# Performance work log

Hardware: AMD Instinct MI355X
Metric: run time of the kernel (lower is better)

Reference implementation:

```python
import jax, jax.numpy as jnp
import numpy as np

N_NODES = 100000
N_EDGES = 1600000
D_IN = 128
D_HID = 128
D_OUT = 10
N_GRAPHS = 512


def _sage_conv(x, src, dst, W_l, b_l, W_r, num_nodes):
    # PyG SAGEConv (mean aggr): out = lin_l(mean_{j in N(i)} x_j) + lin_r(x_i)
    msg = x[src]                                            # [E, D] gather
    s = jax.ops.segment_sum(msg, dst, num_segments=num_nodes)
    cnt = jax.ops.segment_sum(jnp.ones((src.shape[0], 1), x.dtype), dst,
                              num_segments=num_nodes)
    mean = s / jnp.maximum(cnt, 1.0)                        # 0 where no neighbors
    return mean @ W_l.T + b_l + x @ W_r.T


def setup_inputs() -> dict:
    key = jax.random.key(0)
    ks = jax.random.split(key, 10)
    glorot = lambda k, o, i: jax.random.normal(k, (o, i), jnp.float32) * (1.0 / np.sqrt(i))
    return {
        "x": jax.random.normal(ks[0], (N_NODES, D_IN), jnp.float32),
        "edge_index": jax.random.randint(ks[1], (2, N_EDGES), 0, N_NODES, jnp.int64),
        "batch": jnp.sort(jax.random.randint(ks[2], (N_NODES,), 0, N_GRAPHS, jnp.int64)),
        "W1_l": glorot(ks[3], D_HID, D_IN),
        "b1": jnp.zeros((D_HID,), jnp.float32),
        "W1_r": glorot(ks[4], D_HID, D_IN),
        "W2_l": glorot(ks[5], D_HID, D_HID),
        "b2": jnp.zeros((D_HID,), jnp.float32),
        "W2_r": glorot(ks[6], D_HID, D_HID),
        "Wf": glorot(ks[7], D_OUT, D_HID),
        "bf": jnp.zeros((D_OUT,), jnp.float32),
    }


def reference(x, edge_index, batch, W1_l, b1, W1_r, W2_l, b2, W2_r, Wf, bf):
    src, dst = edge_index[0], edge_index[1]
    n = x.shape[0]
    h = jax.nn.relu(_sage_conv(x, src, dst, W1_l, b1, W1_r, n))
    h = jax.nn.relu(_sage_conv(h, src, dst, W2_l, b2, W2_r, n))
    # global_mean_pool over graph ids
    gsum = jax.ops.segment_sum(h, batch, num_segments=N_GRAPHS)
    gcnt = jax.ops.segment_sum(jnp.ones((n, 1), h.dtype), batch, num_segments=N_GRAPHS)
    g = gsum / jnp.maximum(gcnt, 1.0)
    logits = g @ Wf.T + bf
    return jax.nn.log_softmax(logits, axis=-1)
```

## Files before the change

kernel.cpp:

```cpp
#include <hip/hip_runtime.h>
#include <hip/hip_bf16.h>

#define N_NODES 100000
#define N_EDGES 1600000
#define N_GRAPHS 512
#define NB 256
#define NPB 391
#define CHUNK 6250
#define STAGE 7680

typedef __attribute__((ext_vector_type(8))) short short8;
typedef __attribute__((ext_vector_type(4))) float f32x4;
typedef __attribute__((ext_vector_type(2))) float f32x2;

__device__ __forceinline__ float b2f(ushort u) {
    union { unsigned int i; float f; } c; c.i = ((unsigned int)u) << 16; return c.f;
}
__device__ __forceinline__ float blo(unsigned int u) {
    union { unsigned int i; float f; } c; c.i = u << 16; return c.f;
}
__device__ __forceinline__ float bhi(unsigned int u) {
    union { unsigned int i; float f; } c; c.i = u & 0xffff0000u; return c.f;
}
__device__ __forceinline__ ushort f2b(float f) {
    union { float f; unsigned int i; } c; c.f = f;
    unsigned int r = (c.i + 0x7fffu + ((c.i >> 16) & 1u)) >> 16;
    return (ushort)r;
}
__device__ __forceinline__ int idx_at(const void* p, long i, int f) {
    return f ? (int)((const long long*)p)[i] : ((const int*)p)[i];
}

__global__ __launch_bounds__(256) void k_detect(const unsigned int* __restrict__ xw,
                                                const unsigned int* __restrict__ ew,
                                                const int* __restrict__ bw,
                                                int* __restrict__ flags) {
    __shared__ int cf, ce, cb;
    int t = threadIdx.x;
    if (t == 0) { cf = 0; ce = 0; cb = 0; }
    __syncthreads();
    unsigned int w = xw[t];
    unsigned int e = (w >> 7) & 0xffu;
    if (e >= 110u && e <= 130u) atomicAdd(&cf, 1);
    if (t < 128) {
        if (ew[2 * t + 1] != 0u) atomicAdd(&ce, 1);
        if (bw[99001 + 2 * t] != 0) atomicAdd(&cb, 1);
    }
    __syncthreads();
    if (t == 0) {
        flags[0] = (cf >= 128) ? 1 : 0;
        flags[1] = (ce == 0) ? 1 : 0;
        flags[2] = (cb == 0) ? 1 : 0;
    }
}

__global__ __launch_bounds__(256) void k_prep(const void* __restrict__ ei,
                                              const void* __restrict__ x,
                                              ushort* __restrict__ xbf,
                                              unsigned int* __restrict__ xf8,
                                              const void* W1l, const void* W1r,
                                              const void* W2l, const void* W2r,
                                              const void* b1,  const void* b2,
                                              ushort* __restrict__ wbf,
                                              int* __restrict__ blkcnt,
                                              const int* __restrict__ flags) {
    int b = blockIdx.x, t = threadIdx.x;
    if (b < NB) {
        __shared__ int h[NB];
        int f = flags[1];
        for (int j = t; j < NB; j += 256) h[j] = 0;
        __syncthreads();
        int lo = b * CHUNK, hi = lo + CHUNK;
        for (int e = lo + t; e < hi; e += 256) {
            int d = idx_at(ei, (long)N_EDGES + e, f);
            atomicAdd(&h[d / NPB], 1);
        }
        __syncthreads();
        if (t < NB) blkcnt[b * NB + t] = h[t];
    } else if (b < NB + 2048) {
        bool f32src = (flags[0] == 0);
        int vb = b - NB;
        const long nG = (long)N_NODES * 128 / 4;
        for (long g = (long)vb * 256 + t; g < nG; g += 2048L * 256) {
            float v0, v1, v2, v3;
            if (f32src) {
                float4 vv = ((const float4*)x)[g];
                v0 = vv.x; v1 = vv.y; v2 = vv.z; v3 = vv.w;
                unsigned int lo = (unsigned int)f2b(v0) | ((unsigned int)f2b(v1) << 16);
                unsigned int hi = (unsigned int)f2b(v2) | ((unsigned int)f2b(v3) << 16);
                ((uint2*)xbf)[g] = make_uint2(lo, hi);
            } else {
                uint2 q = ((const uint2*)x)[g];
                v0 = blo(q.x); v1 = bhi(q.x); v2 = blo(q.y); v3 = bhi(q.y);
            }
            int r = __builtin_amdgcn_cvt_pk_fp8_f32(v0, v1, 0, false);
            r = __builtin_amdgcn_cvt_pk_fp8_f32(v2, v3, r, true);
            xf8[g] = (unsigned int)r;
        }
    } else {
        int idx = (b - NB - 2048) * 256 + t;
        if (idx >= 65792) return;
        const void* src; int off;
        if      (idx < 16384) { src = W1l; off = idx; }
        else if (idx < 32768) { src = W1r; off = idx - 16384; }
        else if (idx < 49152) { src = W2l; off = idx - 32768; }
        else if (idx < 65536) { src = W2r; off = idx - 49152; }
        else if (idx < 65664) { src = b1;  off = idx - 65536; }
        else                  { src = b2;  off = idx - 65664; }
        wbf[idx] = (flags[0] != 0) ? ((const ushort*)src)[off]
                                   : f2b(((const float*)src)[off]);
    }
}

__global__ __launch_bounds__(NB) void k_bscan(const int* __restrict__ blkcnt,
                                              int* __restrict__ bucketBase,
                                              int* __restrict__ blkbase) {
    __shared__ int s[NB];
    int t = threadIdx.x;
    int tot = 0;
    for (int blk = 0; blk < NB; ++blk) tot += blkcnt[blk * NB + t];
    s[t] = tot; __syncthreads();
    for (int off = 1; off < NB; off <<= 1) {
        int a = (t >= off) ? s[t - off] : 0;
        __syncthreads();
        s[t] += a;
        __syncthreads();
    }
    int excl = s[t] - tot;
    bucketBase[t] = excl;
    if (t == NB - 1) bucketBase[NB] = s[NB - 1];
    int run = excl;
    for (int blk = 0; blk < NB; ++blk) {
        blkbase[blk * NB + t] = run;
        run += blkcnt[blk * NB + t];
    }
}

__global__ __launch_bounds__(256) void k_bin(const void* __restrict__ ei,
                                             const int* __restrict__ blkbase,
                                             int* __restrict__ binned,
                                             const int* __restrict__ flags) {
    __shared__ int bb[NB];
    __shared__ int rank[NB];
    int t = threadIdx.x, blk = blockIdx.x;
    int f = flags[1];
    for (int j = t; j < NB; j += 256) { bb[j] = blkbase[blk * NB + j]; rank[j] = 0; }
    __syncthreads();
    int lo = blk * CHUNK, hi = lo + CHUNK;
    for (int e = lo + t; e < hi; e += 256) {
        int s = idx_at(ei, e, f);
        int d = idx_at(ei, (long)N_EDGES + e, f);
        int b = d / NPB;
        int loc = d - b * NPB;
        int r = atomicAdd(&rank[b], 1);
        binned[bb[b] + r] = s | (loc << 20);
    }
}

__global__ __launch_bounds__(256) void k_csr(const int* __restrict__ binned,
                                             const int* __restrict__ bucketBase,
                                             int* __restrict__ rowptr,
                                             int* __restrict__ csr) {
    __shared__ int cnt[400];
    __shared__ int sc[400];
    __shared__ int sh[256];
    __shared__ int stage[STAGE];
    int t = threadIdx.x, b = blockIdx.x;
    int nodeLo = b * NPB;
    int nC = N_NODES - nodeLo; if (nC > NPB) nC = NPB;
    int eBase = bucketBase[b], eEnd = bucketBase[b + 1];

    for (int j = t; j < 400; j += 256) cnt[j] = 0;
    __syncthreads();
    for (int i = eBase + t; i < eEnd; i += 256)
        atomicAdd(&cnt[binned[i] >> 20], 1);
    __syncthreads();
    int base = t * 2;
    int v0 = (base < 400) ? cnt[base] : 0;
    int v1 = (base + 1 < 400) ? cnt[base + 1] : 0;
    int ssum = v0 + v1;
    sh[t] = ssum; __syncthreads();
    for (int off = 1; off < 256; off <<= 1) {
        int a = (t >= off) ? sh[t - off] : 0;
        __syncthreads();
        sh[t] += a;
        __syncthreads();
    }
    int pre = sh[t] - ssum;
    if (base < 400) sc[base] = pre;
    if (base + 1 < 400) sc[base + 1] = pre + v0;
    __syncthreads();
    for (int j = t; j < nC; j += 256) rowptr[nodeLo + j] = eBase + sc[j];
    if (b == NB - 1) {
        if (t == 0) rowptr[N_NODES] = eEnd;
        if (t < 64) csr[N_EDGES + t] = 0;
    }
    for (int j = t; j < 400; j += 256) cnt[j] = 0;
    __syncthreads();
    for (int i = eBase + t; i < eEnd; i += 256) {
        int p = binned[i];
        int loc = p >> 20;
        int pos = sc[loc] + atomicAdd(&cnt[loc], 1);
        int srcn = p & 0xFFFFF;
        if (pos < STAGE) stage[pos] = srcn;
        else csr[eBase + pos] = srcn;
    }
    __syncthreads();
    int eCnt = eEnd - eBase; if (eCnt > STAGE) eCnt = STAGE;
    for (int j = t; j < eCnt; j += 256) csr[eBase + j] = stage[j];
}

__global__ __launch_bounds__(256) void k_agg(const unsigned int* __restrict__ x32,
                                             const int* __restrict__ rowptr,
                                             const int* __restrict__ csr,
                                             uint2* __restrict__ mout) {
    int wv = blockIdx.x * 4 + (threadIdx.x >> 6);
    int lane = threadIdx.x & 63;
    int li = lane & 31;
    int node = wv * 2 + (lane >> 5);
    if (node >= N_NODES) return;
    int beg = rowptr[node];
    int end = rowptr[node + 1];
    int deg = end - beg;
    int degO = __shfl_xor(deg, 32);
    int degmax = __builtin_amdgcn_readfirstlane(deg > degO ? deg : degO);
    float a0 = 0.f, a1 = 0.f, a2 = 0.f, a3 = 0.f;
    for (int j = 0; j < degmax; j += 32) {
        int pos = beg + j + li;
        if (pos > end - 1) pos = (deg > 0) ? end - 1 : 0;
        int vidx = csr[pos];
#pragma unroll
        for (int c = 0; c < 32; c += 8) {
            if (j + c >= degmax) break;
            unsigned int p[8];
#pragma unroll
            for (int i = 0; i < 8; ++i) {
                int idx = __shfl(vidx, (c + i) | (lane & 32));
                p[i] = x32[(long)idx * 32 + li];
            }
#pragma unroll
            for (int i = 0; i < 8; ++i) {
                unsigned int q = (j + c + i < deg) ? p[i] : 0u;
                f32x2 d0 = __builtin_amdgcn_cvt_pk_f32_fp8((int)q, false);
                f32x2 d1 = __builtin_amdgcn_cvt_pk_f32_fp8((int)q, true);
                a0 += d0.x; a1 += d0.y; a2 += d1.x; a3 += d1.y;
            }
        }
    }
    float scale = (deg > 0) ? 1.f / (float)deg : 0.f;
    unsigned int lo = (unsigned int)f2b(a0 * scale) | ((unsigned int)f2b(a1 * scale) << 16);
    unsigned int hi = (unsigned int)f2b(a2 * scale) | ((unsigned int)f2b(a3 * scale) << 16);
    mout[(long)node * 32 + li] = make_uint2(lo, hi);
}

__global__ __launch_bounds__(256) void k_gemm(const ushort* __restrict__ A0,
                                              const ushort* __restrict__ A1a,
                                              const ushort* __restrict__ A1b,
                                              const uchar* __restrict__ A1f8,
                                              const ushort* __restrict__ Wl,
                                              const ushort* __restrict__ Wr,
                                              const ushort* __restrict__ bias,
                                              ushort* __restrict__ outb,
                                              uchar* __restrict__ out8,
                                              const int* __restrict__ flags,
                                              int layer1) {
    __shared__ short Ws[4096 * 8];
    int t = threadIdx.x;
    const ushort* A1 = flags[0] ? A1a : A1b;
#pragma unroll
    for (int i = 0; i < 16; ++i) {
        int f = i * 256 + t;
        int lane = f & 63, kk = (f >> 6) & 7, tile = f >> 9;
        int o = tile * 16 + (lane & 15);
        int k0 = kk * 32 + ((lane >> 4) * 8);
        const ushort* wsrc = (k0 < 128) ? (Wl + o * 128 + k0)
                                        : (Wr + o * 128 + (k0 - 128));
        *(short8*)&Ws[f * 8] = *(const short8*)wsrc;
    }
    __syncthreads();

    int wid = t >> 6, lane = t & 63;
    long nbase = (long)blockIdx.x * 64 + (long)wid * 16;
    int arow = (int)nbase + (lane & 15);
    if (arow >= N_NODES) arow = N_NODES - 1;
    int kq = (lane >> 4) * 8;

    short8 afrag[8];
#pragma unroll
    for (int kk = 0; kk < 8; ++kk) {
        int k0 = kk * 32 + kq;
        if (k0 < 128) {
            afrag[kk] = *(const short8*)(A0 + (long)arow * 128 + k0);
        } else if (layer1) {
            afrag[kk] = *(const short8*)(A1 + (long)arow * 128 + (k0 - 128));
        } else {
            const uchar* fp = A1f8 + (long)arow * 128 + (k0 - 128);
            uint2 q = *(const uint2*)fp;
            f32x2 d0 = __builtin_amdgcn_cvt_pk_f32_fp8((int)q.x, false);
            f32x2 d1 = __builtin_amdgcn_cvt_pk_f32_fp8((int)q.x, true);
            f32x2 d2 = __builtin_amdgcn_cvt_pk_f32_fp8((int)q.y, false);
            f32x2 d3 = __builtin_amdgcn_cvt_pk_f32_fp8((int)q.y, true);
            short8 s;
            s[0] = (short)f2b(d0.x); s[1] = (short)f2b(d0.y);
            s[2] = (short)f2b(d1.x); s[3] = (short)f2b(d1.y);
            s[4] = (short)f2b(d2.x); s[5] = (short)f2b(d2.y);
            s[6] = (short)f2b(d3.x); s[7] = (short)f2b(d3.y);
            afrag[kk] = s;
        }
    }

#pragma unroll
    for (int tile = 0; tile < 8; ++tile) {
        f32x4 acc = {0.f, 0.f, 0.f, 0.f};
#pragma unroll
        for (int kk = 0; kk < 8; ++kk) {
            short8 bfrag = *(short8*)&Ws[((tile * 8 + kk) * 64 + lane) * 8];
            acc = __builtin_amdgcn_mfma_f32_16x16x32_bf16(afrag[kk], bfrag, acc, 0, 0, 0);
        }
        int o = tile * 16 + (lane & 15);
        float bo = b2f(bias[o]);
#pragma unroll
        for (int r = 0; r < 4; ++r) {
            long node = nbase + (lane >> 4) * 4 + r;
            if (node < N_NODES) {
                float v = acc[r] + bo;
                v = v > 0.f ? v : 0.f;
                if (layer1) {
                    int pp = __builtin_amdgcn_cvt_pk_fp8_f32(v, v, 0, false);
                    out8[node * 128 + o] = (uchar)pp;
                } else {
                    outb[node * 128 + o] = f2b(v);
                }
            }
        }
    }
}

__global__ __launch_bounds__(256) void k_pool_cls(const ushort* __restrict__ h2,
                                                  const void* __restrict__ batch,
                                                  const void* __restrict__ Wf,
                                                  const void* __restrict__ bfv,
                                                  void* __restrict__ outp,
                                                  const int* __restrict__ flags) {
    int g = blockIdx.x, t = threadIdx.x;
    int wid = t >> 6, lane = t & 63;
    bool f32 = (flags[0] == 0);
    int b64 = flags[2];
    __shared__ int rng[2];
    __shared__ float redA[4][64];
    __shared__ float redB[4][64];
    __shared__ float gv[128];
    __shared__ float lg[10];
    if (t < 2) {
        int v = g + t, lo = 0, hi = N_NODES;
        while (lo < hi) {
            int mid = (lo + hi) >> 1;
            if (idx_at(batch, mid, b64) < v) lo = mid + 1; else hi = mid;
        }
        rng[t] = lo;
    }
    __syncthreads();
    int lo = rng[0], hi = rng[1];
    const unsigned int* xr = (const unsigned int*)h2;
    float a0 = 0.f, a1 = 0.f;
    int n = lo + wid;
    for (; n + 28 < hi; n += 32) {
        unsigned int p[8];
#pragma unroll
        for (int i = 0; i < 8; ++i) p[i] = xr[(long)(n + i * 4) * 64 + lane];
#pragma unroll
        for (int i = 0; i < 8; ++i) { a0 += blo(p[i]); a1 += bhi(p[i]); }
    }
    for (; n < hi; n += 4) {
        unsigned int q = xr[(long)n * 64 + lane];
        a0 += blo(q); a1 += bhi(q);
    }
    redA[wid][lane] = a0;
    redB[wid][lane] = a1;
    __syncthreads();
    if (wid == 0) {
        float s0 = redA[0][lane] + redA[1][lane] + redA[2][lane] + redA[3][lane];
        float s1 = redB[0][lane] + redB[1][lane] + redB[2][lane] + redB[3][lane];
        float c = (hi > lo) ? (float)(hi - lo) : 1.f;
        gv[lane * 2]     = s0 / c;
        gv[lane * 2 + 1] = s1 / c;
    }
    __syncthreads();
    if (t < 10) {
        float s = f32 ? ((const float*)bfv)[t] : b2f(((const ushort*)bfv)[t]);
        for (int k = 0; k < 128; ++k) {
            float wv = f32 ? ((const float*)Wf)[t * 128 + k] : b2f(((const ushort*)Wf)[t * 128 + k]);
            s += gv[k] * wv;
        }
        lg[t] = s;
    }
    __syncthreads();
    if (t == 0) {
        float mx = lg[0];
        for (int i = 1; i < 10; ++i) mx = fmaxf(mx, lg[i]);
        float se = 0.f;
        for (int i = 0; i < 10; ++i) se += expf(lg[i] - mx);
        float lse = mx + logf(se);
        for (int i = 0; i < 10; ++i) {
            float v = lg[i] - lse;
            if (f32) ((float*)outp)[g * 10 + i] = v;
            else     ((ushort*)outp)[g * 10 + i] = f2b(v);
        }
    }
}

extern "C" void kernel_launch(void* const* d_in, const int* in_sizes, int n_in,
                              void* d_out, int out_size, void* d_ws, size_t ws_size,
                              hipStream_t stream) {
    const void* x     = d_in[0];
    const void* ei    = d_in[1];
    const void* batch = d_in[2];
    const void* W1l = d_in[3];
    const void* b1  = d_in[4];
    const void* W1r = d_in[5];
    const void* W2l = d_in[6];
    const void* b2  = d_in[7];
    const void* W2r = d_in[8];
    const void* Wf  = d_in[9];
    const void* bf_ = d_in[10];

    char* w = (char*)d_ws;
    int* flags      = (int*)(w + 0);
    int* rowptr     = (int*)(w + 640);
    ushort* wbf     = (ushort*)(w + 400768);
    int* csr        = (int*)(w + 532480);
    ushort* xbf     = (ushort*)(w + 6933248);
    ushort* mbuf    = (ushort*)(w + 32533248);
    int* bucketBase = (int*)(w + 32533248);
    int* blkcnt     = (int*)(w + 32534528);
    int* blkbase    = (int*)(w + 32796672);
    uchar* h1f8     = (uchar*)(w + 58133248);
    int* binned     = (int*)(w + 58133248);
    unsigned int* xf8 = (unsigned int*)(w + 70933248);
    ushort* h2      = mbuf;

    dim3 blk256(256), blkNB(NB);

    k_detect<<<1, blk256, 0, stream>>>((const unsigned int*)x, (const unsigned int*)ei,
                                       (const int*)batch, flags);
    k_prep<<<NB + 2048 + 257, blk256, 0, stream>>>(ei, x, xbf, xf8,
                                                   W1l, W1r, W2l, W2r, b1, b2,
                                                   wbf, blkcnt, flags);
    k_bscan<<<1, blkNB, 0, stream>>>(blkcnt, bucketBase, blkbase);
    k_bin<<<NB, blk256, 0, stream>>>(ei, blkbase, binned, flags);
    k_csr<<<NB, blk256, 0, stream>>>(binned, bucketBase, rowptr, csr);

    int agrid = (N_NODES / 2 + 3) / 4;
    int ggrid = (N_NODES + 63) / 64;

    k_agg<<<agrid, blk256, 0, stream>>>(xf8, rowptr, csr, (uint2*)mbuf);
    k_gemm<<<ggrid, blk256, 0, stream>>>(mbuf, (const ushort*)x, xbf, (const uchar*)nullptr,
                                         wbf + 0, wbf + 16384, wbf + 65536,
                                         (ushort*)nullptr, h1f8, flags, 1);
    k_agg<<<agrid, blk256, 0, stream>>>((const unsigned int*)h1f8, rowptr, csr, (uint2*)mbuf);
    k_gemm<<<ggrid, blk256, 0, stream>>>(mbuf, (const ushort*)x, xbf, h1f8,
                                         wbf + 32768, wbf + 49152, wbf + 65664,
                                         h2, (uchar*)nullptr, flags, 0);
    k_pool_cls<<<N_GRAPHS, blk256, 0, stream>>>(h2, batch, Wf, bf_, d_out, flags);
}
```

Measured before the change: 330.5 us.

## Store aggregated means as FP8 and use 16 lanes per node in aggregation

The aggregation kernel now assigns 16 lanes per node (four nodes per wave), each lane gathering 8 FP8 bytes instead of 4. The mean output is written as FP8 instead of BF16, which halves its write and read traffic. The GEMM decodes it with a shared FP8-to-BF16 helper. h2 is relocated into the xbf region so it no longer aliases the FP8 mean buffer. The cost is extra precision loss on the aggregated means, and degree-imbalance divergence now spans four nodes per wave instead of two.

```diff
diff --git a/kernel.cpp b/kernel.cpp
--- a/kernel.cpp
+++ b/kernel.cpp
@@ -29,6 +29,19 @@
 }
 __device__ __forceinline__ int idx_at(const void* p, long i, int f) {
     return f ? (int)((const long long*)p)[i] : ((const int*)p)[i];
+}
+__device__ __forceinline__ short8 dec8(const uchar* p) {
+    uint2 q = *(const uint2*)p;
+    f32x2 d0 = __builtin_amdgcn_cvt_pk_f32_fp8((int)q.x, false);
+    f32x2 d1 = __builtin_amdgcn_cvt_pk_f32_fp8((int)q.x, true);
+    f32x2 d2 = __builtin_amdgcn_cvt_pk_f32_fp8((int)q.y, false);
+    f32x2 d3 = __builtin_amdgcn_cvt_pk_f32_fp8((int)q.y, true);
+    short8 s;
+    s[0] = (short)f2b(d0.x); s[1] = (short)f2b(d0.y);
+    s[2] = (short)f2b(d1.x); s[3] = (short)f2b(d1.y);
+    s[4] = (short)f2b(d2.x); s[5] = (short)f2b(d2.y);
+    s[6] = (short)f2b(d3.x); s[7] = (short)f2b(d3.y);
+    return s;
 }
 
 __global__ __launch_bounds__(256) void k_detect(const unsigned int* __restrict__ xw,
@@ -210,50 +223,59 @@
     for (int j = t; j < eCnt; j += 256) csr[eBase + j] = stage[j];
 }
 
-__global__ __launch_bounds__(256) void k_agg(const unsigned int* __restrict__ x32,
+__global__ __launch_bounds__(256) void k_agg(const uint2* __restrict__ x16,
                                              const int* __restrict__ rowptr,
                                              const int* __restrict__ csr,
                                              uint2* __restrict__ mout) {
     int wv = blockIdx.x * 4 + (threadIdx.x >> 6);
     int lane = threadIdx.x & 63;
-    int li = lane & 31;
-    int node = wv * 2 + (lane >> 5);
-    if (node >= N_NODES) return;
+    int li = lane & 15;
+    int node = wv * 4 + (lane >> 4);
     int beg = rowptr[node];
     int end = rowptr[node + 1];
     int deg = end - beg;
-    int degO = __shfl_xor(deg, 32);
-    int degmax = __builtin_amdgcn_readfirstlane(deg > degO ? deg : degO);
+    int m = deg;
+    m = max(m, __shfl_xor(m, 16));
+    m = max(m, __shfl_xor(m, 32));
+    int degmax = __builtin_amdgcn_readfirstlane(m);
     float a0 = 0.f, a1 = 0.f, a2 = 0.f, a3 = 0.f;
-    for (int j = 0; j < degmax; j += 32) {
+    float a4 = 0.f, a5 = 0.f, a6 = 0.f, a7 = 0.f;
+    for (int j = 0; j < degmax; j += 16) {
         int pos = beg + j + li;
         if (pos > end - 1) pos = (deg > 0) ? end - 1 : 0;
         int vidx = csr[pos];
 #pragma unroll
-        for (int c = 0; c < 32; c += 8) {
+        for (int c = 0; c < 16; c += 8) {
             if (j + c >= degmax) break;
-            unsigned int p[8];
+            uint2 p[8];
 #pragma unroll
             for (int i = 0; i < 8; ++i) {
-                int idx = __shfl(vidx, (c + i) | (lane & 32));
-                p[i] = x32[(long)idx * 32 + li];
+                int idx = __shfl(vidx, (c + i) | (lane & 48));
+                p[i] = x16[(long)idx * 16 + li];
             }
 #pragma unroll
             for (int i = 0; i < 8; ++i) {
-                unsigned int q = (j + c + i < deg) ? p[i] : 0u;
-                f32x2 d0 = __builtin_amdgcn_cvt_pk_f32_fp8((int)q, false);
-                f32x2 d1 = __builtin_amdgcn_cvt_pk_f32_fp8((int)q, true);
+                bool ok = (j + c + i < deg);
+                unsigned int qx = ok ? p[i].x : 0u;
+                unsigned int qy = ok ? p[i].y : 0u;
+                f32x2 d0 = __builtin_amdgcn_cvt_pk_f32_fp8((int)qx, false);
+                f32x2 d1 = __builtin_amdgcn_cvt_pk_f32_fp8((int)qx, true);
+                f32x2 d2 = __builtin_amdgcn_cvt_pk_f32_fp8((int)qy, false);
+                f32x2 d3 = __builtin_amdgcn_cvt_pk_f32_fp8((int)qy, true);
                 a0 += d0.x; a1 += d0.y; a2 += d1.x; a3 += d1.y;
+                a4 += d2.x; a5 += d2.y; a6 += d3.x; a7 += d3.y;
             }
         }
     }
-    float scale = (deg > 0) ? 1.f / (float)deg : 0.f;
-    unsigned int lo = (unsigned int)f2b(a0 * scale) | ((unsigned int)f2b(a1 * scale) << 16);
-    unsigned int hi = (unsigned int)f2b(a2 * scale) | ((unsigned int)f2b(a3 * scale) << 16);
-    mout[(long)node * 32 + li] = make_uint2(lo, hi);
-}
-
-__global__ __launch_bounds__(256) void k_gemm(const ushort* __restrict__ A0,
+    float s = (deg > 0) ? 1.f / (float)deg : 0.f;
+    int r0 = __builtin_amdgcn_cvt_pk_fp8_f32(a0 * s, a1 * s, 0, false);
+    r0 = __builtin_amdgcn_cvt_pk_fp8_f32(a2 * s, a3 * s, r0, true);
+    int r1 = __builtin_amdgcn_cvt_pk_fp8_f32(a4 * s, a5 * s, 0, false);
+    r1 = __builtin_amdgcn_cvt_pk_fp8_f32(a6 * s, a7 * s, r1, true);
+    mout[(long)node * 16 + li] = make_uint2((unsigned int)r0, (unsigned int)r1);
+}
+
+__global__ __launch_bounds__(256) void k_gemm(const uchar* __restrict__ A0f8,
                                               const ushort* __restrict__ A1a,
                                               const ushort* __restrict__ A1b,
                                               const uchar* __restrict__ A1f8,
@@ -290,22 +312,11 @@
     for (int kk = 0; kk < 8; ++kk) {
         int k0 = kk * 32 + kq;
         if (k0 < 128) {
-            afrag[kk] = *(const short8*)(A0 + (long)arow * 128 + k0);
+            afrag[kk] = dec8(A0f8 + (long)arow * 128 + k0);
         } else if (layer1) {
             afrag[kk] = *(const short8*)(A1 + (long)arow * 128 + (k0 - 128));
         } else {
-            const uchar* fp = A1f8 + (long)arow * 128 + (k0 - 128);
-            uint2 q = *(const uint2*)fp;
-            f32x2 d0 = __builtin_amdgcn_cvt_pk_f32_fp8((int)q.x, false);
-            f32x2 d1 = __builtin_amdgcn_cvt_pk_f32_fp8((int)q.x, true);
-            f32x2 d2 = __builtin_amdgcn_cvt_pk_f32_fp8((int)q.y, false);
-            f32x2 d3 = __builtin_amdgcn_cvt_pk_f32_fp8((int)q.y, true);
-            short8 s;
-            s[0] = (short)f2b(d0.x); s[1] = (short)f2b(d0.y);
-            s[2] = (short)f2b(d1.x); s[3] = (short)f2b(d1.y);
-            s[4] = (short)f2b(d2.x); s[5] = (short)f2b(d2.y);
-            s[6] = (short)f2b(d3.x); s[7] = (short)f2b(d3.y);
-            afrag[kk] = s;
+            afrag[kk] = dec8(A1f8 + (long)arow * 128 + (k0 - 128));
         }
     }
 
@@ -430,14 +441,14 @@
     ushort* wbf     = (ushort*)(w + 400768);
     int* csr        = (int*)(w + 532480);
     ushort* xbf     = (ushort*)(w + 6933248);
-    ushort* mbuf    = (ushort*)(w + 32533248);
+    ushort* h2      = (ushort*)(w + 6933248);
+    uchar* mbuf     = (uchar*)(w + 32533248);
     int* bucketBase = (int*)(w + 32533248);
     int* blkcnt     = (int*)(w + 32534528);
     int* blkbase    = (int*)(w + 32796672);
     uchar* h1f8     = (uchar*)(w + 58133248);
     int* binned     = (int*)(w + 58133248);
     unsigned int* xf8 = (unsigned int*)(w + 70933248);
-    ushort* h2      = mbuf;
 
     dim3 blk256(256), blkNB(NB);
 
@@ -450,14 +461,14 @@
     k_bin<<<NB, blk256, 0, stream>>>(ei, blkbase, binned, flags);
     k_csr<<<NB, blk256, 0, stream>>>(binned, bucketBase, rowptr, csr);
 
-    int agrid = (N_NODES / 2 + 3) / 4;
+    int agrid = N_NODES / 4 / 4;
     int ggrid = (N_NODES + 63) / 64;
 
-    k_agg<<<agrid, blk256, 0, stream>>>(xf8, rowptr, csr, (uint2*)mbuf);
+    k_agg<<<agrid, blk256, 0, stream>>>((const uint2*)xf8, rowptr, csr, (uint2*)mbuf);
     k_gemm<<<ggrid, blk256, 0, stream>>>(mbuf, (const ushort*)x, xbf, (const uchar*)nullptr,
                                          wbf + 0, wbf + 16384, wbf + 65536,
                                          (ushort*)nullptr, h1f8, flags, 1);
-    k_agg<<<agrid, blk256, 0, stream>>>((const unsigned int*)h1f8, rowptr, csr, (uint2*)mbuf);
+    k_agg<<<agrid, blk256, 0, stream>>>((const uint2*)h1f8, rowptr, csr, (uint2*)mbuf);
     k_gemm<<<ggrid, blk256, 0, stream>>>(mbuf, (const ushort*)x, xbf, h1f8,
                                          wbf + 32768, wbf + 49152, wbf + 65664,
                                          h2, (uchar*)nullptr, flags, 0);
```

Result: faster. 319.4 us (-3.3%).
